# Kernel tuning notes

Hardware: AMD Instinct MI355X
Metric: run time of the kernel (lower is better)

Reference implementation:

```python
import jax, jax.numpy as jnp
import numpy as np

B, N, K, CIN, COUT, H = 4, 2048, 32, 16, 32, 32
EPS = 1e-5


def setup_inputs() -> dict:
    key = jax.random.key(0)
    ks = jax.random.split(key, 6)
    s = 0.1
    return dict(
        xyz=jax.random.uniform(ks[0], (B, N, 3), dtype=jnp.float32),
        points=jax.random.normal(ks[1], (B, N, CIN), dtype=jnp.float32),
        W1=jax.random.normal(ks[2], (3, H), dtype=jnp.float32) * s,
        b1=jnp.zeros((H,), jnp.float32),
        g1=jnp.ones((H,), jnp.float32),
        be1=jnp.zeros((H,), jnp.float32),
        W2=jax.random.normal(ks[3], (H, H), dtype=jnp.float32) * s,
        b2=jnp.zeros((H,), jnp.float32),
        g2=jnp.ones((H,), jnp.float32),
        be2=jnp.zeros((H,), jnp.float32),
        W3=jax.random.normal(ks[4], (H, CIN * COUT), dtype=jnp.float32) * s,
        b3=jnp.zeros((CIN * COUT,), jnp.float32),
        gbn=jnp.ones((COUT,), jnp.float32),
        bbn=jnp.zeros((COUT,), jnp.float32),
    )


def _bn(h, g, b):
    # BatchNorm1d training-mode math: biased batch stats over axis 0
    return g * (h - h.mean(0)) / jnp.sqrt(h.var(0) + EPS) + b


def reference(xyz, points, W1, b1, g1, be1, W2, b2, g2, be2, W3, b3, gbn, bbn):
    # KNN: squared distances (B,N,N)
    sq = jnp.sum(xyz * xyz, -1)
    dist = -2.0 * jnp.einsum('bmc,bnc->bmn', xyz, xyz) + sq[:, :, None] + sq[:, None, :]
    _, idx = jax.lax.top_k(-dist, K)  # (B,N,K) nearest neighbors

    gather = jax.vmap(lambda p, i: p[i])  # (N,C),(N,K)->(N,K,C), vmapped over B
    grouped_xyz = gather(xyz, idx)                      # (B,N,K,3)
    rel = grouped_xyz - xyz[:, :, None, :]              # (B,N,K,3)
    grouped_pts = gather(points, idx)                   # (B,N,K,CIN)

    # weight net on relative coords
    h = rel.reshape(-1, 3)
    h = _bn(jax.nn.relu(h @ W1 + b1), g1, be1)
    h = _bn(jax.nn.relu(h @ W2 + b2), g2, be2)
    w = (h @ W3 + b3).reshape(B, N, K, CIN, COUT)       # (B,N,K,CIN,COUT)

    # weighted sum over C_in, then max over neighbors
    out = jnp.einsum('bnkc,bnkco->bnko', grouped_pts, w)  # (B,N,K,COUT)
    out = out.max(axis=2)                                 # (B,N,COUT)

    # final BatchNorm1d over (B,N) per channel
    m = out.mean((0, 1))
    v = out.var((0, 1))
    return gbn * (out - m) / jnp.sqrt(v + EPS) + bbn
```

## Files before the change

### kernel.cpp

```cpp
#include <hip/hip_runtime.h>

#define B_ 4
#define N_ 2048
#define K_ 32
#define CIN_ 16
#define COUT_ 32
#define H_ 32
#define R_ (B_*N_*K_)
#define EPS_ 1e-5f
#define INVR_ (1.0f/(float)R_)
#define INVBN_ (1.0f/(float)(B_*N_))
#define LISTCAP 112
#define NSH 16

typedef __attribute__((ext_vector_type(8)))  _Float16 f16x8;
typedef __attribute__((ext_vector_type(2)))  __fp16   hw16x2;
typedef __attribute__((ext_vector_type(2)))  _Float16 f16x2;
typedef __attribute__((ext_vector_type(16))) float    f32x16;

__device__ __forceinline__ float dot3f(float ax,float ay,float az,float bx,float by,float bz){
    return fmaf(az,bz, fmaf(ay,by, ax*bx));
}
__device__ __forceinline__ unsigned int pk2(float a, float b){
    union { hw16x2 v; unsigned int u; } c;
    c.v = __builtin_amdgcn_cvt_pkrtz(a, b);
    return c.u;
}
__device__ __forceinline__ unsigned int pkmul(unsigned int a, unsigned int b){
    union { unsigned int u; f16x2 v; } x, y, r;
    x.u = a; y.u = b; r.v = x.v * y.v; return r.u;
}
__device__ __forceinline__ float shsum(const float* __restrict__ p, int k){
    float s = 0.f;
    #pragma unroll
    for (int i = 0; i < NSH; ++i) s += p[i*32 + k];
    return s;
}

__global__ __launch_bounds__(256) void k_prep0(const float* __restrict__ xyz, float4* __restrict__ xs4g,
                                               float* __restrict__ st){
    int i = blockIdx.x*256 + threadIdx.x;
    float x = xyz[3*i], y = xyz[3*i+1], z = xyz[3*i+2];
    xs4g[i] = make_float4(x, y, z, dot3f(x,y,z,x,y,z));
    if (blockIdx.x == 0){
        for (int j = threadIdx.x; j < 1152; j += 256) st[j] = 0.f;
    }
}

__global__ __launch_bounds__(256,6) void k_knn(const float4* __restrict__ xs4g,
                                               const float* __restrict__ W1, const float* __restrict__ b1,
                                               int* __restrict__ idx_out,
                                               float* __restrict__ s1sh, float* __restrict__ q1sh){
    __shared__ unsigned int hist[4][512][2];
    __shared__ unsigned long long lst[4][LISTCAP];
    __shared__ int kidx[4][K_];

    const int tid  = threadIdx.x;
    const int w    = tid >> 6;
    const int lane = tid & 63;
    const int half = lane >> 5;
    const int b    = blockIdx.x >> 9;
    const int q    = ((blockIdx.x & 511) << 2) + w;
    const int bN   = b * N_;
    unsigned int* hw = &hist[w][0][0];

    const uint4 z4 = make_uint4(0,0,0,0);
    uint4* h4 = (uint4*)hw;
    #pragma unroll
    for (int i = 0; i < 4; ++i) h4[i*64 + lane] = z4;

    const float4 qp = xs4g[bN + q];
    const float qx = qp.x, qy = qp.y, qz = qp.z, sqq = qp.w;

    unsigned int fv[32];
    #pragma unroll
    for (int j = 0; j < 32; ++j){
        int c = j*64 + lane;
        float4 pt = xs4g[bN + c];
        float d = fmaf(-2.0f, dot3f(qx,qy,qz, pt.x,pt.y,pt.z), sqq) + pt.w;
        fv[j] = __float_as_uint(d);
        unsigned int u1 = __float_as_uint(d + 1.0f);
        unsigned int key = (u1 <= 0x3F800000u) ? 0u : ((u1 - 0x3F800000u) >> 15);
        key = key > 511u ? 511u : key;
        atomicAdd(&hw[key*2 + (lane & 1)], 1u);
    }

    unsigned int g[8];
    #pragma unroll
    for (int t = 0; t < 4; ++t){
        uint4 h = ((const uint4*)hw)[lane*4 + t];
        g[2*t]   = h.x + h.y;
        g[2*t+1] = h.z + h.w;
    }
    unsigned int gs = 0;
    #pragma unroll
    for (int t = 0; t < 8; ++t) gs += g[t];
    unsigned int cum = gs;
    #pragma unroll
    for (int off = 1; off < 64; off <<= 1){
        unsigned int v = __shfl_up(cum, off);
        if (lane >= off) cum += v;
    }
    unsigned long long bal = __ballot(cum >= (unsigned)K_);
    int L = __ffsll(bal) - 1;
    unsigned int run = __shfl(cum, L) - __shfl(gs, L);
    int Bsel = 8*L + 7;
    {
        unsigned int c = run; bool fnd = false;
        #pragma unroll
        for (int t = 0; t < 8; ++t){
            unsigned int ht = __shfl(g[t], L, 64);
            if (!fnd && c + ht >= (unsigned)K_){ Bsel = 8*L + t; fnd = true; }
            c += ht;
        }
    }
    const float Tedge = __uint_as_float(0x3F800000u + ((unsigned)(Bsel + 1) << 15));
    const bool allin = (Bsel == 511);

    const unsigned long long mlt = (lane == 63) ? ~0ull >> 1 : (1ull << lane) - 1ull;
    unsigned int cnt = 0;
    #pragma unroll
    for (int j = 0; j < 32; ++j){
        float f1 = __uint_as_float(fv[j]) + 1.0f;
        bool surv = (f1 < Tedge) || allin;
        unsigned long long sb = __ballot(surv);
        unsigned int pos = cnt + (unsigned int)__popcll(sb & mlt);
        if (surv && pos < (unsigned)LISTCAP)
            lst[w][pos] = ((unsigned long long)fv[j] << 32) | (unsigned int)(j*64 + lane);
        cnt += (unsigned int)__popcll(sb);
    }
    int m = (int)cnt; if (m > LISTCAP) m = LISTCAP;

    int* outp = idx_out + ((size_t)bN + q) * K_;
    for (int i = lane; i < m; i += 64){
        unsigned long long my = lst[w][i];
        int rank = 0;
        for (int jj = 0; jj < m; ++jj)
            rank += (lst[w][jj] < my) ? 1 : 0;
        if (rank < K_){
            int id = (int)(unsigned int)(my & 0xFFFFFFFFull);
            outp[rank] = id;
            kidx[w][rank] = id;
        }
    }

    {
        const int ch = lane & 31;
        float w1a = W1[ch], w1b = W1[H_+ch], w1c = W1[2*H_+ch], b1c = b1[ch];
        float s = 0.f, qq = 0.f;
        #pragma unroll
        for (int r = 0; r < 16; ++r){
            int idr = kidx[w][half*16 + r];
            float4 pn = xs4g[bN + idr];
            float rx = pn.x - qx, ry = pn.y - qy, rz = pn.z - qz;
            float h = fmaxf(fmaf(rx, w1a, fmaf(ry, w1b, fmaf(rz, w1c, b1c))), 0.0f);
            s += h; qq = fmaf(h, h, qq);
        }
        s  += __shfl_xor(s, 32, 64);
        qq += __shfl_xor(qq, 32, 64);
        if (lane < 32){
            int sh = (blockIdx.x & (NSH-1)) * 32 + ch;
            atomicAdd(&s1sh[sh], s);
            atomicAdd(&q1sh[sh], qq);
        }
    }
}

__device__ __forceinline__ void compute_h1v(const float4* __restrict__ xs4g, const int* __restrict__ idx, int r,
                                            const float* __restrict__ W1, const float* __restrict__ b1, float* h1){
    int b = r >> 16;
    int n = (r >> 5) & (N_-1);
    int id = idx[r];
    float4 pc = xs4g[b*N_ + n];
    float4 pn = xs4g[b*N_ + id];
    float rx = pn.x - pc.x, ry = pn.y - pc.y, rz = pn.z - pc.z;
    #pragma unroll
    for (int j = 0; j < H_; ++j){
        float a = fmaf(rx, W1[j], fmaf(ry, W1[H_+j], fmaf(rz, W1[2*H_+j], b1[j])));
        h1[j] = fmaxf(a, 0.0f);
    }
}

__global__ __launch_bounds__(256) void k_prep2(const float* __restrict__ points,
                                               const float* __restrict__ s1s, const float* __restrict__ q1s,
                                               const float* __restrict__ g1, const float* __restrict__ be1,
                                               const float* __restrict__ W2, const float* __restrict__ b2,
                                               unsigned int* __restrict__ pf16, unsigned int* __restrict__ W2f,
                                               float* __restrict__ b2p){
    int flat = blockIdx.x*256 + threadIdx.x;
    if (flat < 65536){
        pf16[flat] = pk2(points[2*flat], points[2*flat+1]);
    } else if (flat < 66048){
        int d = flat - 65536;
        int jj = d & 3, lane = (d >> 2) & 63, s = d >> 8;
        int col = lane & 31;
        int k0 = s*16 + (lane >> 5)*8 + 2*jj;
        float m0 = shsum(s1s,k0)*INVR_,   v0 = shsum(q1s,k0)*INVR_   - m0*m0;
        float m1 = shsum(s1s,k0+1)*INVR_, v1 = shsum(q1s,k0+1)*INVR_ - m1*m1;
        float a0  = g1[k0]   / sqrtf(v0 + EPS_);
        float a1v = g1[k0+1] / sqrtf(v1 + EPS_);
        W2f[d] = pk2(a0*W2[k0*H_ + col], a1v*W2[(k0+1)*H_ + col]);
    } else if (flat < 66080){
        int col = flat - 66048;
        float acc = b2[col];
        #pragma unroll 4
        for (int h = 0; h < H_; ++h){
            float mm = shsum(s1s,h)*INVR_, vv = shsum(q1s,h)*INVR_ - mm*mm;
            float aa = g1[h] / sqrtf(vv + EPS_);
            float bb = fmaf(-aa, mm, be1[h]);
            acc = fmaf(bb, W2[h*H_ + col], acc);
        }
        b2p[col] = acc;
    }
}

__global__ __launch_bounds__(256,4) void k_h2stats(const float4* __restrict__ xs4g, const int* __restrict__ idx,
                                                   const float* __restrict__ W1, const float* __restrict__ b1,
                                                   const uint4* __restrict__ W2f, const float* __restrict__ b2p,
                                                   float* gsum, float* gsq){
    __shared__ float redS[H_], redQ[H_];
    const int tid = threadIdx.x, lane = tid & 63, w = tid >> 6;
    const int half = lane >> 5, m = lane & 31;
    if (tid < H_){ redS[tid] = 0.f; redQ[tid] = 0.f; }
    __syncthreads();

    int r = blockIdx.x*256 + tid;
    float h1[H_];
    compute_h1v(xs4g, idx, r, W1, b1, h1);
    unsigned int h1p[16];
    #pragma unroll
    for (int i = 0; i < 16; ++i) h1p[i] = pk2(h1[2*i], h1[2*i+1]);

    union { uint4 u4; f16x8 v; } Bf0, Bf1;
    Bf0.u4 = W2f[lane];
    Bf1.u4 = W2f[64 + lane];
    float b2c = b2p[m];

    float s = 0.f, q = 0.f;
    #pragma unroll
    for (int t = 0; t < 2; ++t){
        const int src = t*32 + m;
        union { unsigned int u[4]; f16x8 v; } a0, a1f;
        #pragma unroll
        for (int jj = 0; jj < 4; ++jj){
            unsigned int lo = __shfl(h1p[jj],     src, 64);
            unsigned int hi = __shfl(h1p[4 + jj], src, 64);
            a0.u[jj] = half ? hi : lo;
        }
        #pragma unroll
        for (int jj = 0; jj < 4; ++jj){
            unsigned int lo = __shfl(h1p[8 + jj],  src, 64);
            unsigned int hi = __shfl(h1p[12 + jj], src, 64);
            a1f.u[jj] = half ? hi : lo;
        }
        f32x16 acc;
        #pragma unroll
        for (int i = 0; i < 16; ++i) acc[i] = b2c;
        acc = __builtin_amdgcn_mfma_f32_32x32x16_f16(a0.v,  Bf0.v, acc, 0, 0, 0);
        acc = __builtin_amdgcn_mfma_f32_32x32x16_f16(a1f.v, Bf1.v, acc, 0, 0, 0);
        #pragma unroll
        for (int i = 0; i < 16; ++i){
            float v = fmaxf(acc[i], 0.0f);
            s += v; q = fmaf(v, v, q);
        }
    }
    s += __shfl_xor(s, 32, 64);
    q += __shfl_xor(q, 32, 64);
    if (lane < 32){ atomicAdd(&redS[m], s); atomicAdd(&redQ[m], q); }
    __syncthreads();
    if (tid < H_){ atomicAdd(&gsum[tid], redS[tid]); atomicAdd(&gsq[tid], redQ[tid]); }
}

__global__ __launch_bounds__(256) void k_prep3(const float* __restrict__ W3, const float* __restrict__ b3,
                                               const float* __restrict__ s2, const float* __restrict__ q2,
                                               const float* __restrict__ g2, const float* __restrict__ be2,
                                               unsigned int* __restrict__ W3f){
    int d = blockIdx.x*256 + threadIdx.x;
    int jj = d & 3, lane = (d >> 2) & 63, step = d >> 8;
    int col = lane & 31;
    int off = (lane >> 5)*8 + 2*jj;
    float v0, v1;
    if (step < 32){
        int h = step, c0 = off;
        float mm = s2[h]*INVR_, vv = q2[h]*INVR_ - mm*mm;
        float aa = g2[h] / sqrtf(vv + EPS_);
        v0 = aa * W3[h*512 + c0*COUT_ + col];
        v1 = aa * W3[h*512 + (c0+1)*COUT_ + col];
    } else {
        int c0 = off;
        v0 = b3[c0*COUT_ + col]; v1 = b3[(c0+1)*COUT_ + col];
        #pragma unroll 4
        for (int h = 0; h < H_; ++h){
            float mm = s2[h]*INVR_, vv = q2[h]*INVR_ - mm*mm;
            float aa = g2[h] / sqrtf(vv + EPS_);
            float bb = fmaf(-aa, mm, be2[h]);
            v0 = fmaf(bb, W3[h*512 + c0*COUT_ + col], v0);
            v1 = fmaf(bb, W3[h*512 + (c0+1)*COUT_ + col], v1);
        }
    }
    W3f[d] = pk2(v0, v1);
}

__global__ __launch_bounds__(256,3) void k_out(const float4* __restrict__ xs4g, const int* __restrict__ idx,
                                               const float* __restrict__ W1, const float* __restrict__ b1,
                                               const uint4* __restrict__ W2f, const float* __restrict__ b2p,
                                               const unsigned int* __restrict__ pf16,
                                               const uint4* __restrict__ W3f,
                                               float* __restrict__ out_pre, float* gsum, float* gsq){
    __shared__ float redS[COUT_], redQ[COUT_];
    const int tid = threadIdx.x, lane = tid & 63, w = tid >> 6;
    const int half = lane >> 5, m = lane & 31;
    if (tid < COUT_){ redS[tid] = 0.f; redQ[tid] = 0.f; }
    __syncthreads();

    const int rB = blockIdx.x*256 + w*64;
    int r = blockIdx.x*256 + tid;

    float h1[H_];
    compute_h1v(xs4g, idx, r, W1, b1, h1);
    unsigned int h1p[16];
    #pragma unroll
    for (int i = 0; i < 16; ++i) h1p[i] = pk2(h1[2*i], h1[2*i+1]);

    union { uint4 u4; f16x8 v; } A0, A1;
    A0.u4 = W2f[lane];
    A1.u4 = W2f[64 + lane];
    float b2v[16];
    #pragma unroll
    for (int i = 0; i < 16; ++i) b2v[i] = b2p[(i&3) + 8*(i>>2) + 4*half];

    const uint4* Wf = W3f + lane;

    #pragma unroll
    for (int t = 0; t < 2; ++t){
        const int src = t*32 + m;
        union { unsigned int u[4]; f16x8 v; } B0f, B1f;
        #pragma unroll
        for (int jj = 0; jj < 4; ++jj){
            unsigned int lo = __shfl(h1p[jj],     src, 64);
            unsigned int hi = __shfl(h1p[4 + jj], src, 64);
            B0f.u[jj] = half ? hi : lo;
        }
        #pragma unroll
        for (int jj = 0; jj < 4; ++jj){
            unsigned int lo = __shfl(h1p[8 + jj],  src, 64);
            unsigned int hi = __shfl(h1p[12 + jj], src, 64);
            B1f.u[jj] = half ? hi : lo;
        }
        f32x16 c2;
        #pragma unroll
        for (int i = 0; i < 16; ++i) c2[i] = b2v[i];
        c2 = __builtin_amdgcn_mfma_f32_32x32x16_f16(A0.v, B0f.v, c2, 0, 0, 0);
        c2 = __builtin_amdgcn_mfma_f32_32x32x16_f16(A1.v, B1f.v, c2, 0, 0, 0);

        unsigned int h2p[16];
        #pragma unroll
        for (int p = 0; p < 8; ++p){
            float v0 = fmaxf(c2[2*p],   0.0f);
            float v1 = fmaxf(c2[2*p+1], 0.0f);
            unsigned int ow = pk2(v0, v1);
            unsigned int ot = __shfl_xor(ow, 32, 64);
            int a = p >> 1, bb = p & 1;
            h2p[4*a + 2*half     + bb] = ow;
            h2p[4*a + 2*(1-half) + bb] = ot;
        }

        int row = rB + t*32 + m;
        int bb_ = row >> 16;
        int idr = idx[row];
        const uint4* gpp = (const uint4*)(pf16 + ((size_t)bb_*N_ + idr)*8);
        uint4 ga = gpp[0], gb = gpp[1];
        unsigned int gsel[4];
        gsel[0] = half ? gb.x : ga.x;
        gsel[1] = half ? gb.y : ga.y;
        gsel[2] = half ? gb.z : ga.z;
        gsel[3] = half ? gb.w : ga.w;

        f32x16 acc;
        #pragma unroll
        for (int i = 0; i < 16; ++i) acc[i] = 0.f;
        #pragma unroll
        for (int kb = 0; kb < 32; ++kb){
            unsigned int hr = h2p[kb >> 1];
            unsigned int hd = __builtin_amdgcn_perm(hr, hr, (kb & 1) ? 0x03020302u : 0x01000100u);
            union { unsigned int u[4]; f16x8 v; } af;
            #pragma unroll
            for (int jj = 0; jj < 4; ++jj) af.u[jj] = pkmul(hd, gsel[jj]);
            union { uint4 u4; f16x8 v; } bf; bf.u4 = Wf[kb*64];
            acc = __builtin_amdgcn_mfma_f32_32x32x16_f16(af.v, bf.v, acc, 0, 0, 0);
        }
        {
            union { unsigned int u[4]; f16x8 v; } af;
            #pragma unroll
            for (int jj = 0; jj < 4; ++jj) af.u[jj] = gsel[jj];
            union { uint4 u4; f16x8 v; } bf; bf.u4 = Wf[32*64];
            acc = __builtin_amdgcn_mfma_f32_32x32x16_f16(af.v, bf.v, acc, 0, 0, 0);
        }

        float v = acc[0];
        #pragma unroll
        for (int i = 1; i < 16; ++i) v = fmaxf(v, acc[i]);
        v = fmaxf(v, __shfl_xor(v, 32, 64));
        if (lane < 32){
            int g = blockIdx.x*8 + w*2 + t;
            out_pre[(size_t)g*COUT_ + m] = v;
            atomicAdd(&redS[m], v);
            atomicAdd(&redQ[m], v*v);
        }
    }
    __syncthreads();
    if (tid < COUT_){ atomicAdd(&gsum[tid], redS[tid]); atomicAdd(&gsq[tid], redQ[tid]); }
}

__global__ __launch_bounds__(256) void k_bn(const float* __restrict__ out_pre,
                                            const float* __restrict__ s3, const float* __restrict__ q3,
                                            const float* __restrict__ gbn, const float* __restrict__ bbn,
                                            float* __restrict__ out){
    int i = blockIdx.x*256 + threadIdx.x;
    int o = i & (COUT_-1);
    float mm = s3[o] * INVBN_;
    float vv = q3[o] * INVBN_ - mm*mm;
    float aa = gbn[o] / sqrtf(vv + EPS_);
    out[i] = fmaf(aa, out_pre[i], fmaf(-aa, mm, bbn[o]));
}

extern "C" void kernel_launch(void* const* d_in, const int* in_sizes, int n_in,
                              void* d_out, int out_size, void* d_ws, size_t ws_size,
                              hipStream_t stream){
    const float* xyz    = (const float*)d_in[0];
    const float* points = (const float*)d_in[1];
    const float* W1  = (const float*)d_in[2];
    const float* b1  = (const float*)d_in[3];
    const float* g1  = (const float*)d_in[4];
    const float* be1 = (const float*)d_in[5];
    const float* W2  = (const float*)d_in[6];
    const float* b2  = (const float*)d_in[7];
    const float* g2  = (const float*)d_in[8];
    const float* be2 = (const float*)d_in[9];
    const float* W3  = (const float*)d_in[10];
    const float* b3  = (const float*)d_in[11];
    const float* gbn = (const float*)d_in[12];
    const float* bbn = (const float*)d_in[13];
    float* out = (float*)d_out;

    char* base = (char*)d_ws;
    int*            idx     = (int*)(base + 0);
    float*          out_pre = (float*)(base + 1048576);
    unsigned int*   pf16    = (unsigned int*)(base + 2097152);
    unsigned int*   W3f     = (unsigned int*)(base + 2359296);
    unsigned int*   W2f     = (unsigned int*)(base + 2393088);
    float*          b2p     = (float*)(base + 2395136);
    float*          st      = (float*)(base + 2395264);
    float4*         xs4g    = (float4*)(base + 2399872);
    float *s1s=st, *q1s=st+512, *s2=st+1024, *q2=st+1056, *s3=st+1088, *q3=st+1120;

    hipLaunchKernelGGL(k_prep0,   dim3(32),      dim3(256), 0, stream, xyz, xs4g, st);
    hipLaunchKernelGGL(k_knn,     dim3(B_*N_/4), dim3(256), 0, stream, xs4g, W1, b1, idx, s1s, q1s);
    hipLaunchKernelGGL(k_prep2,   dim3(260),     dim3(256), 0, stream, points, s1s, q1s, g1, be1, W2, b2,
                       pf16, W2f, b2p);
    hipLaunchKernelGGL(k_h2stats, dim3(R_/256),  dim3(256), 0, stream, xs4g, idx, W1, b1,
                       (const uint4*)W2f, b2p, s2, q2);
    hipLaunchKernelGGL(k_prep3,   dim3(33),      dim3(256), 0, stream, W3, b3, s2, q2, g2, be2, W3f);
    hipLaunchKernelGGL(k_out,     dim3(R_/256),  dim3(256), 0, stream, xs4g, idx, W1, b1,
                       (const uint4*)W2f, b2p, pf16, (const uint4*)W3f, out_pre, s3, q3);
    hipLaunchKernelGGL(k_bn,      dim3(B_*N_*COUT_/256), dim3(256), 0, stream, out_pre, s3, q3, gbn, bbn, out);
}
```

Baseline: 176.1 us.

## Fold prep kernels into neighbors via per-block W2 build and last-block W3 prep

Removes the k_prep2 and k_prep3 launches. Point fp16 packing moves into k_prep0. Every block of k_h2stats and k_out now rebuilds the BN1-folded W2 fragments and bias in shared memory. The last block of k_h2stats, found through an atomic counter, builds the BN2-folded W3 fragments. This cuts two kernel launches and their serialization gaps, at the cost of redundant per-block W2 work, extra syncs, and a tail where a single block does the W3 prep.

```diff
diff --git a/kernel.cpp b/kernel.cpp
--- a/kernel.cpp
+++ b/kernel.cpp
@@ -37,13 +37,17 @@
     return s;
 }
 
-__global__ __launch_bounds__(256) void k_prep0(const float* __restrict__ xyz, float4* __restrict__ xs4g,
+__global__ __launch_bounds__(256) void k_prep0(const float* __restrict__ xyz, const float* __restrict__ points,
+                                               float4* __restrict__ xs4g, unsigned int* __restrict__ pf16,
                                                float* __restrict__ st){
     int i = blockIdx.x*256 + threadIdx.x;
-    float x = xyz[3*i], y = xyz[3*i+1], z = xyz[3*i+2];
-    xs4g[i] = make_float4(x, y, z, dot3f(x,y,z,x,y,z));
+    pf16[i] = pk2(points[2*i], points[2*i+1]);
+    if (i < 8192){
+        float x = xyz[3*i], y = xyz[3*i+1], z = xyz[3*i+2];
+        xs4g[i] = make_float4(x, y, z, dot3f(x,y,z,x,y,z));
+    }
     if (blockIdx.x == 0){
-        for (int j = threadIdx.x; j < 1152; j += 256) st[j] = 0.f;
+        for (int j = threadIdx.x; j < 1280; j += 256) st[j] = 0.f;
     }
 }
 
@@ -181,48 +185,55 @@
     }
 }
 
-__global__ __launch_bounds__(256) void k_prep2(const float* __restrict__ points,
-                                               const float* __restrict__ s1s, const float* __restrict__ q1s,
-                                               const float* __restrict__ g1, const float* __restrict__ be1,
-                                               const float* __restrict__ W2, const float* __restrict__ b2,
-                                               unsigned int* __restrict__ pf16, unsigned int* __restrict__ W2f,
-                                               float* __restrict__ b2p){
-    int flat = blockIdx.x*256 + threadIdx.x;
-    if (flat < 65536){
-        pf16[flat] = pk2(points[2*flat], points[2*flat+1]);
-    } else if (flat < 66048){
-        int d = flat - 65536;
+__device__ __forceinline__ void build_w2f(const float* __restrict__ s1s, const float* __restrict__ q1s,
+                                          const float* __restrict__ g1, const float* __restrict__ be1,
+                                          const float* __restrict__ W2, const float* __restrict__ b2,
+                                          uint4* W2fs, float* b2ps, float* aa1, float* bb1){
+    const int tid = threadIdx.x;
+    if (tid < H_){
+        float mm = shsum(s1s, tid)*INVR_;
+        float vv = shsum(q1s, tid)*INVR_ - mm*mm;
+        float a = g1[tid] / sqrtf(vv + EPS_);
+        aa1[tid] = a;
+        bb1[tid] = fmaf(-a, mm, be1[tid]);
+    }
+    __syncthreads();
+    unsigned int* w2d = (unsigned int*)W2fs;
+    #pragma unroll
+    for (int rep = 0; rep < 2; ++rep){
+        int d = tid + rep*256;
         int jj = d & 3, lane = (d >> 2) & 63, s = d >> 8;
         int col = lane & 31;
         int k0 = s*16 + (lane >> 5)*8 + 2*jj;
-        float m0 = shsum(s1s,k0)*INVR_,   v0 = shsum(q1s,k0)*INVR_   - m0*m0;
-        float m1 = shsum(s1s,k0+1)*INVR_, v1 = shsum(q1s,k0+1)*INVR_ - m1*m1;
-        float a0  = g1[k0]   / sqrtf(v0 + EPS_);
-        float a1v = g1[k0+1] / sqrtf(v1 + EPS_);
-        W2f[d] = pk2(a0*W2[k0*H_ + col], a1v*W2[(k0+1)*H_ + col]);
-    } else if (flat < 66080){
-        int col = flat - 66048;
-        float acc = b2[col];
+        w2d[d] = pk2(aa1[k0]*W2[k0*H_ + col], aa1[k0+1]*W2[(k0+1)*H_ + col]);
+    }
+    if (tid < H_){
+        float acc = b2[tid];
         #pragma unroll 4
-        for (int h = 0; h < H_; ++h){
-            float mm = shsum(s1s,h)*INVR_, vv = shsum(q1s,h)*INVR_ - mm*mm;
-            float aa = g1[h] / sqrtf(vv + EPS_);
-            float bb = fmaf(-aa, mm, be1[h]);
-            acc = fmaf(bb, W2[h*H_ + col], acc);
-        }
-        b2p[col] = acc;
-    }
+        for (int h = 0; h < H_; ++h) acc = fmaf(bb1[h], W2[h*H_ + tid], acc);
+        b2ps[tid] = acc;
+    }
+    __syncthreads();
 }
 
 __global__ __launch_bounds__(256,4) void k_h2stats(const float4* __restrict__ xs4g, const int* __restrict__ idx,
                                                    const float* __restrict__ W1, const float* __restrict__ b1,
-                                                   const uint4* __restrict__ W2f, const float* __restrict__ b2p,
-                                                   float* gsum, float* gsq){
+                                                   const float* __restrict__ s1s, const float* __restrict__ q1s,
+                                                   const float* __restrict__ g1, const float* __restrict__ be1,
+                                                   const float* __restrict__ W2, const float* __restrict__ b2,
+                                                   const float* __restrict__ g2, const float* __restrict__ be2,
+                                                   const float* __restrict__ W3, const float* __restrict__ b3,
+                                                   float* gsum, float* gsq,
+                                                   unsigned int* __restrict__ ctr,
+                                                   unsigned int* __restrict__ W3f){
+    __shared__ uint4 W2fs[128];
+    __shared__ float b2ps[H_], aa1[H_], bb1[H_];
     __shared__ float redS[H_], redQ[H_];
-    const int tid = threadIdx.x, lane = tid & 63, w = tid >> 6;
+    __shared__ int lastf;
+    const int tid = threadIdx.x, lane = tid & 63;
     const int half = lane >> 5, m = lane & 31;
     if (tid < H_){ redS[tid] = 0.f; redQ[tid] = 0.f; }
-    __syncthreads();
+    build_w2f(s1s, q1s, g1, be1, W2, b2, W2fs, b2ps, aa1, bb1);
 
     int r = blockIdx.x*256 + tid;
     float h1[H_];
@@ -232,9 +243,9 @@
     for (int i = 0; i < 16; ++i) h1p[i] = pk2(h1[2*i], h1[2*i+1]);
 
     union { uint4 u4; f16x8 v; } Bf0, Bf1;
-    Bf0.u4 = W2f[lane];
-    Bf1.u4 = W2f[64 + lane];
-    float b2c = b2p[m];
+    Bf0.u4 = W2fs[lane];
+    Bf1.u4 = W2fs[64 + lane];
+    float b2c = b2ps[m];
 
     float s = 0.f, q = 0.f;
     #pragma unroll
@@ -269,49 +280,60 @@
     if (lane < 32){ atomicAdd(&redS[m], s); atomicAdd(&redQ[m], q); }
     __syncthreads();
     if (tid < H_){ atomicAdd(&gsum[tid], redS[tid]); atomicAdd(&gsq[tid], redQ[tid]); }
-}
-
-__global__ __launch_bounds__(256) void k_prep3(const float* __restrict__ W3, const float* __restrict__ b3,
-                                               const float* __restrict__ s2, const float* __restrict__ q2,
-                                               const float* __restrict__ g2, const float* __restrict__ be2,
-                                               unsigned int* __restrict__ W3f){
-    int d = blockIdx.x*256 + threadIdx.x;
-    int jj = d & 3, lane = (d >> 2) & 63, step = d >> 8;
-    int col = lane & 31;
-    int off = (lane >> 5)*8 + 2*jj;
-    float v0, v1;
-    if (step < 32){
-        int h = step, c0 = off;
-        float mm = s2[h]*INVR_, vv = q2[h]*INVR_ - mm*mm;
-        float aa = g2[h] / sqrtf(vv + EPS_);
-        v0 = aa * W3[h*512 + c0*COUT_ + col];
-        v1 = aa * W3[h*512 + (c0+1)*COUT_ + col];
-    } else {
-        int c0 = off;
-        v0 = b3[c0*COUT_ + col]; v1 = b3[(c0+1)*COUT_ + col];
-        #pragma unroll 4
-        for (int h = 0; h < H_; ++h){
-            float mm = s2[h]*INVR_, vv = q2[h]*INVR_ - mm*mm;
-            float aa = g2[h] / sqrtf(vv + EPS_);
-            float bb = fmaf(-aa, mm, be2[h]);
-            v0 = fmaf(bb, W3[h*512 + c0*COUT_ + col], v0);
-            v1 = fmaf(bb, W3[h*512 + (c0+1)*COUT_ + col], v1);
-        }
-    }
-    W3f[d] = pk2(v0, v1);
+
+    __syncthreads();
+    if (tid == 0){
+        __threadfence();
+        lastf = (atomicAdd(ctr, 1u) == (unsigned)gridDim.x - 1u) ? 1 : 0;
+    }
+    __syncthreads();
+    if (lastf){
+        __shared__ float aa2[H_], bb2[H_];
+        if (tid < H_){
+            float sv = __hip_atomic_load(&gsum[tid], __ATOMIC_RELAXED, __HIP_MEMORY_SCOPE_AGENT);
+            float qv = __hip_atomic_load(&gsq[tid],  __ATOMIC_RELAXED, __HIP_MEMORY_SCOPE_AGENT);
+            float mm = sv*INVR_, vv = qv*INVR_ - mm*mm;
+            float a = g2[tid] / sqrtf(vv + EPS_);
+            aa2[tid] = a;
+            bb2[tid] = fmaf(-a, mm, be2[tid]);
+        }
+        __syncthreads();
+        for (int d = tid; d < 8448; d += 256){
+            int jj = d & 3, lane2 = (d >> 2) & 63, step = d >> 8;
+            int col = lane2 & 31;
+            int off = (lane2 >> 5)*8 + 2*jj;
+            float v0, v1;
+            if (step < 32){
+                v0 = aa2[step] * W3[step*512 + off*COUT_ + col];
+                v1 = aa2[step] * W3[step*512 + (off+1)*COUT_ + col];
+            } else {
+                v0 = b3[off*COUT_ + col]; v1 = b3[(off+1)*COUT_ + col];
+                #pragma unroll 4
+                for (int h = 0; h < H_; ++h){
+                    v0 = fmaf(bb2[h], W3[h*512 + off*COUT_ + col], v0);
+                    v1 = fmaf(bb2[h], W3[h*512 + (off+1)*COUT_ + col], v1);
+                }
+            }
+            W3f[d] = pk2(v0, v1);
+        }
+    }
 }
 
 __global__ __launch_bounds__(256,3) void k_out(const float4* __restrict__ xs4g, const int* __restrict__ idx,
                                                const float* __restrict__ W1, const float* __restrict__ b1,
-                                               const uint4* __restrict__ W2f, const float* __restrict__ b2p,
+                                               const float* __restrict__ s1s, const float* __restrict__ q1s,
+                                               const float* __restrict__ g1, const float* __restrict__ be1,
+                                               const float* __restrict__ W2, const float* __restrict__ b2,
                                                const unsigned int* __restrict__ pf16,
                                                const uint4* __restrict__ W3f,
                                                float* __restrict__ out_pre, float* gsum, float* gsq){
+    __shared__ uint4 W2fs[128];
+    __shared__ float b2ps[H_], aa1[H_], bb1[H_];
     __shared__ float redS[COUT_], redQ[COUT_];
     const int tid = threadIdx.x, lane = tid & 63, w = tid >> 6;
     const int half = lane >> 5, m = lane & 31;
     if (tid < COUT_){ redS[tid] = 0.f; redQ[tid] = 0.f; }
-    __syncthreads();
+    build_w2f(s1s, q1s, g1, be1, W2, b2, W2fs, b2ps, aa1, bb1);
 
     const int rB = blockIdx.x*256 + w*64;
     int r = blockIdx.x*256 + tid;
@@ -323,11 +345,11 @@
     for (int i = 0; i < 16; ++i) h1p[i] = pk2(h1[2*i], h1[2*i+1]);
 
     union { uint4 u4; f16x8 v; } A0, A1;
-    A0.u4 = W2f[lane];
-    A1.u4 = W2f[64 + lane];
+    A0.u4 = W2fs[lane];
+    A1.u4 = W2fs[64 + lane];
     float b2v[16];
     #pragma unroll
-    for (int i = 0; i < 16; ++i) b2v[i] = b2p[(i&3) + 8*(i>>2) + 4*half];
+    for (int i = 0; i < 16; ++i) b2v[i] = b2ps[(i&3) + 8*(i>>2) + 4*half];
 
     const uint4* Wf = W3f + lane;
 
@@ -448,20 +470,16 @@
     float*          out_pre = (float*)(base + 1048576);
     unsigned int*   pf16    = (unsigned int*)(base + 2097152);
     unsigned int*   W3f     = (unsigned int*)(base + 2359296);
-    unsigned int*   W2f     = (unsigned int*)(base + 2393088);
-    float*          b2p     = (float*)(base + 2395136);
-    float*          st      = (float*)(base + 2395264);
-    float4*         xs4g    = (float4*)(base + 2399872);
+    float*          st      = (float*)(base + 2393088);
+    float4*         xs4g    = (float4*)(base + 2398208);
     float *s1s=st, *q1s=st+512, *s2=st+1024, *q2=st+1056, *s3=st+1088, *q3=st+1120;
-
-    hipLaunchKernelGGL(k_prep0,   dim3(32),      dim3(256), 0, stream, xyz, xs4g, st);
+    unsigned int* ctr = (unsigned int*)(st + 1152);
+
+    hipLaunchKernelGGL(k_prep0,   dim3(256),     dim3(256), 0, stream, xyz, points, xs4g, pf16, st);
     hipLaunchKernelGGL(k_knn,     dim3(B_*N_/4), dim3(256), 0, stream, xs4g, W1, b1, idx, s1s, q1s);
-    hipLaunchKernelGGL(k_prep2,   dim3(260),     dim3(256), 0, stream, points, s1s, q1s, g1, be1, W2, b2,
-                       pf16, W2f, b2p);
     hipLaunchKernelGGL(k_h2stats, dim3(R_/256),  dim3(256), 0, stream, xs4g, idx, W1, b1,
-                       (const uint4*)W2f, b2p, s2, q2);
-    hipLaunchKernelGGL(k_prep3,   dim3(33),      dim3(256), 0, stream, W3, b3, s2, q2, g2, be2, W3f);
+                       s1s, q1s, g1, be1, W2, b2, g2, be2, W3, b3, s2, q2, ctr, W3f);
     hipLaunchKernelGGL(k_out,     dim3(R_/256),  dim3(256), 0, stream, xs4g, idx, W1, b1,
-                       (const uint4*)W2f, b2p, pf16, (const uint4*)W3f, out_pre, s3, q3);
+                       s1s, q1s, g1, be1, W2, b2, pf16, (const uint4*)W3f, out_pre, s3, q3);
     hipLaunchKernelGGL(k_bn,      dim3(B_*N_*COUT_/256), dim3(256), 0, stream, out_pre, s3, q3, gbn, bbn, out);
 }
```

Result: slower. 204.9 us (+16.4%).
